# Performance work log

Measured on AMD Instinct MI355X. Metric: run time of the kernel, lower is better.

The kernel has to match this reference:

```python
import jax, jax.numpy as jnp
import numpy as np

N = 50000      # nodes
E = 800000     # edges
IN = 256       # in_feats
H = 128        # out_classes*2
OUT = 64       # out_classes
ALPHA = 0.3


def setup_inputs() -> dict:
    key = jax.random.key(0)
    ks = jax.random.split(key, 12)
    x = jax.random.normal(ks[0], (N, IN), jnp.float32)
    edge_index = jax.random.randint(ks[1], (2, E), 0, N, dtype=jnp.int32)
    def lin(k, fi, fo):
        s = 1.0 / np.float32(np.sqrt(fi))
        kw, kb = jax.random.split(k)
        return (jax.random.uniform(kw, (fi, fo), jnp.float32, -s, s),
                jax.random.uniform(kb, (fo,), jnp.float32, -s, s))
    W1, b1 = lin(ks[2], IN, H)
    W2, b2 = lin(ks[3], H, H)
    W3, b3 = lin(ks[4], H, H)
    Wfc, bfc = lin(ks[5], H, OUT)
    jk_weights = jax.random.normal(ks[6], (3,), jnp.float32)
    return dict(x=x, edge_index=edge_index, W1=W1, b1=b1, W2=W2, b2=b2,
                W3=W3, b3=b3, jk_weights=jk_weights, Wfc=Wfc, bfc=bfc)


def _gcn(x, W, b, src, dst, norm, n):
    # symmetric-normalized GCN conv with self-loops folded into src/dst/norm
    h = x @ W
    return jax.ops.segment_sum(norm[:, None] * h[src], dst, num_segments=n) + b


def reference(x, edge_index, W1, b1, W2, b2, W3, b3, jk_weights, Wfc, bfc):
    n = x.shape[0]
    row, col = edge_index[0], edge_index[1]
    loops = jnp.arange(n, dtype=edge_index.dtype)
    src = jnp.concatenate([row, loops])
    dst = jnp.concatenate([col, loops])
    deg = jax.ops.segment_sum(jnp.ones(src.shape, jnp.float32), dst, num_segments=n)
    dinv = jax.lax.rsqrt(jnp.maximum(deg, 1.0))  # deg >= 1 due to self-loops
    norm = dinv[src] * dinv[dst]

    layer_out = []
    # layer 0 + neighbor sampling (defaults make it exact out-neighbor mean)
    h = jax.nn.relu(_gcn(x, W1, b1, src, dst, norm, n))
    odeg = jax.ops.segment_sum(jnp.ones(row.shape, jnp.float32), row, num_segments=n)
    nsum = jax.ops.segment_sum(h[col], row, num_segments=n)
    h = jnp.where(odeg[:, None] > 0, nsum / jnp.maximum(odeg, 1.0)[:, None], h)
    layer_out.append(h)

    # layer 1 + historical EMA (fresh hist = detached x -> value identity, grad*alpha)
    h = jax.nn.relu(_gcn(h, W2, b2, src, dst, norm, n))
    sg = jax.lax.stop_gradient(h)
    h = sg + ALPHA * (h - sg)
    layer_out.append(h)

    # layer 2
    h = jax.nn.relu(_gcn(h, W3, b3, src, dst, norm, n))
    layer_out.append(h)

    w = jax.nn.softmax(jk_weights)
    jk = w[0] * layer_out[0] + w[1] * layer_out[1] + w[2] * layer_out[2]
    return jk @ Wfc + bfc
```

## Files before the change

### kernel.cpp

```cpp
#include <hip/hip_runtime.h>
#include <hip/hip_bf16.h>


#define H_FEATS 128

typedef __attribute__((ext_vector_type(8))) short short8;
typedef __attribute__((ext_vector_type(4))) float float4v;
typedef unsigned short u16;

__device__ __forceinline__ float dload(const void* p, size_t i, int isbf) {
    return isbf ? __bfloat162float(((const __hip_bfloat16*)p)[i])
                : ((const float*)p)[i];
}

__device__ __forceinline__ float4 load4bf(const u16* p) {
    uint2 u = *(const uint2*)p;
    float4 f;
    f.x = __uint_as_float((u.x & 0xFFFFu) << 16);
    f.y = __uint_as_float(u.x & 0xFFFF0000u);
    f.z = __uint_as_float((u.y & 0xFFFFu) << 16);
    f.w = __uint_as_float(u.y & 0xFFFF0000u);
    return f;
}

__device__ __forceinline__ float bf2f(u16 h) {
    return __uint_as_float((unsigned)h << 16);
}

__device__ __forceinline__ u16 f2bf(float v) {
    return __bfloat16_as_ushort(__float2bfloat16(v));
}

__device__ __forceinline__ void sniff_body(const unsigned int* __restrict__ x,
                                           const void* __restrict__ jkwb,
                                           float* __restrict__ meta) {
    __shared__ int cnt[256];
    int t = threadIdx.x;
    int c = 0;
    for (int i = 0; i < 16; i++) {
        unsigned int w = x[t * 16 + i];
        unsigned int e = (w >> 7) & 0xFFu;
        c += (e >= 0x60u && e <= 0x8Fu) ? 1 : 0;
    }
    cnt[t] = c;
    __syncthreads();
    for (int s = 128; s > 0; s >>= 1) {
        if (t < s) cnt[t] += cnt[t + s];
        __syncthreads();
    }
    if (t == 0) {
        int isbf = (cnt[0] > 3000) ? 1 : 0;
        ((int*)meta)[0] = isbf;
        float w0 = dload(jkwb, 0, isbf);
        float w1 = dload(jkwb, 1, isbf);
        float w2 = dload(jkwb, 2, isbf);
        float m = fmaxf(w0, fmaxf(w1, w2));
        float e0 = expf(w0 - m), e1 = expf(w1 - m), e2 = expf(w2 - m);
        float s = e0 + e1 + e2;
        meta[8] = e0 / s; meta[9] = e1 / s; meta[10] = e2 / s;
    }
}

__global__ __launch_bounds__(256) void sniff_jkw(const unsigned int* __restrict__ x,
                                                 const void* __restrict__ jkwb,
                                                 float* __restrict__ meta) {
    sniff_body(x, jkwb, meta);
}


#define CSR_CH 64
#define CSR_SL 8
#define CSR_NSC (CSR_CH * CSR_SL * 2)

__global__ __launch_bounds__(256) void count_partial(const int* __restrict__ row,
                                                     const int* __restrict__ col,
                                                     unsigned* __restrict__ partC,
                                                     unsigned* __restrict__ partR,
                                                     int E, int N,
                                                     const unsigned int* __restrict__ x,
                                                     const void* __restrict__ jkwb,
                                                     float* __restrict__ meta) {
    if (blockIdx.x == gridDim.x - 1) {
        sniff_body(x, jkwb, meta);
        return;
    }
    int b = blockIdx.x;
    int dir = b >> 9;
    int r = b & 511;
    int sl = r >> 6;
    int k  = r & 63;
    const int* arr = dir ? row : col;
    unsigned* part = (dir ? partR : partC) + (size_t)k * N;
    int lo = (int)(((long long)N * sl) >> 3);
    int hi = (int)(((long long)N * (sl + 1)) >> 3);
    int wid = hi - lo;

    __shared__ unsigned cnt[8192];
    for (int i = threadIdx.x; i < wid; i += 256) cnt[i] = 0;
    __syncthreads();

    int e0 = (int)(((long long)E * k) >> 6);
    int e1 = (int)(((long long)E * (k + 1)) >> 6);
    for (int e = e0 + threadIdx.x; e < e1; e += 256) {
        int d = arr[e] - lo;
        if ((unsigned)d < (unsigned)wid) atomicAdd(&cnt[d], 1u);
    }
    __syncthreads();
    for (int i = threadIdx.x; i < wid; i += 256) part[lo + i] = cnt[i];
}

__global__ __launch_bounds__(256) void reduce_bsum(const unsigned* __restrict__ partC,
                                                   const unsigned* __restrict__ partR,
                                                   int* __restrict__ cntc,
                                                   int* __restrict__ cntr,
                                                   int* __restrict__ b0,
                                                   int* __restrict__ b1, int N) {
    const unsigned* p = blockIdx.y ? partR : partC;
    int* cnt = blockIdx.y ? cntr : cntc;
    int* bs = blockIdx.y ? b1 : b0;
    int base = blockIdx.x * 1024 + threadIdx.x * 4;
    unsigned v0 = 0, v1 = 0, v2 = 0, v3 = 0;
    if (base + 3 < N) {
        for (int k = 0; k < CSR_CH; k++) {
            uint4 u = *(const uint4*)(p + (size_t)k * N + base);
            v0 += u.x; v1 += u.y; v2 += u.z; v3 += u.w;
        }
        int4 w = {(int)v0, (int)v1, (int)v2, (int)v3};
        *(int4*)&cnt[base] = w;
    } else {
        unsigned vv[4] = {0, 0, 0, 0};
        for (int k = 0; k < CSR_CH; k++)
            for (int i = 0; i < 4; i++)
                if (base + i < N) vv[i] += p[(size_t)k * N + base + i];
        for (int i = 0; i < 4; i++) if (base + i < N) cnt[base + i] = (int)vv[i];
        v0 = vv[0]; v1 = vv[1]; v2 = vv[2]; v3 = vv[3];
    }
    int s = (int)(v0 + v1 + v2 + v3);
    __shared__ int red[256];
    red[threadIdx.x] = s;
    __syncthreads();
    for (int d = 128; d > 0; d >>= 1) {
        if (threadIdx.x < d) red[threadIdx.x] += red[threadIdx.x + d];
        __syncthreads();
    }
    if (threadIdx.x == 0) bs[blockIdx.x] = red[0];
}

__global__ __launch_bounds__(256) void prefix_partials(unsigned* __restrict__ partC,
                                                       unsigned* __restrict__ partR,
                                                       const int* __restrict__ coff,
                                                       const int* __restrict__ roff, int N) {
    int i = blockIdx.x * 256 + threadIdx.x;
    if (i >= N) return;
    unsigned* p = blockIdx.y ? partR : partC;
    const int* off = blockIdx.y ? roff : coff;
    unsigned acc = (unsigned)off[i];
    for (int k = 0; k < CSR_CH; k++) {
        unsigned t = p[(size_t)k * N + i];
        p[(size_t)k * N + i] = acc;
        acc += t;
    }
}

__device__ __forceinline__ void scatter_body(int b,
                                             const int* __restrict__ row,
                                             const int* __restrict__ col,
                                             const unsigned* __restrict__ partC,
                                             const unsigned* __restrict__ partR,
                                             u16* __restrict__ ecol,
                                             u16* __restrict__ erow,
                                             int E, int N,
                                             unsigned* __restrict__ cur) {
    int dir = b >> 9;
    int r = b & 511;
    int sl = r >> 6;
    int k  = r & 63;
    const int* darr = dir ? row : col;
    const int* sarr = dir ? col : row;
    u16* out = dir ? erow : ecol;
    const unsigned* base = (dir ? partR : partC) + (size_t)k * N;
    int lo = (int)(((long long)N * sl) >> 3);
    int hi = (int)(((long long)N * (sl + 1)) >> 3);
    int wid = hi - lo;

    for (int i = threadIdx.x; i < wid; i += 256) cur[i] = base[lo + i];
    __syncthreads();

    int e0 = (int)(((long long)E * k) >> 6);
    int e1 = (int)(((long long)E * (k + 1)) >> 6);
    for (int e = e0 + threadIdx.x; e < e1; e += 256) {
        int d = darr[e] - lo;
        if ((unsigned)d < (unsigned)wid) {
            unsigned p = atomicAdd(&cur[d], 1u);
            out[p] = (u16)sarr[e];
        }
    }
}

__global__ __launch_bounds__(256) void histo_sniff(const int* __restrict__ row, const int* __restrict__ col,
                                                   int* __restrict__ cntc, int* __restrict__ cntr, int E,
                                                   const unsigned int* __restrict__ x,
                                                   const void* __restrict__ jkwb,
                                                   float* __restrict__ meta) {
    if (blockIdx.x == gridDim.x - 1) {
        sniff_body(x, jkwb, meta);
        return;
    }
    int e = blockIdx.x * 256 + threadIdx.x;
    if (e < E) {
        atomicAdd(&cntc[col[e]], 1);
        atomicAdd(&cntr[row[e]], 1);
    }
}

__global__ __launch_bounds__(256) void scan_bsum(const int* __restrict__ c0, const int* __restrict__ c1,
                                                 int* __restrict__ b0, int* __restrict__ b1, int N) {
    const int* cnt = blockIdx.y ? c1 : c0;
    int* bs = blockIdx.y ? b1 : b0;
    int base = blockIdx.x * 1024 + threadIdx.x * 4;
    int s = 0;
    if (base + 3 < N) {
        int4 v = *(const int4*)&cnt[base];
        s = v.x + v.y + v.z + v.w;
    } else {
        for (int i = 0; i < 4; i++) if (base + i < N) s += cnt[base + i];
    }
    __shared__ int red[256];
    red[threadIdx.x] = s;
    __syncthreads();
    for (int d = 128; d > 0; d >>= 1) {
        if (threadIdx.x < d) red[threadIdx.x] += red[threadIdx.x + d];
        __syncthreads();
    }
    if (threadIdx.x == 0) bs[blockIdx.x] = red[0];
}

__global__ __launch_bounds__(256) void scan_bsum_scan(int* __restrict__ b0, int* __restrict__ b1,
                                                      int* __restrict__ offN0, int* __restrict__ offN1,
                                                      int nb) {
    int* bs = blockIdx.x ? b1 : b0;
    int* offN = blockIdx.x ? offN1 : offN0;
    __shared__ int sh[256];
    int t = threadIdx.x;
    int v = (t < nb) ? bs[t] : 0;
    sh[t] = v;
    __syncthreads();
    for (int d = 1; d < 256; d <<= 1) {
        int u = (t >= d) ? sh[t - d] : 0;
        __syncthreads();
        sh[t] += u;
        __syncthreads();
    }
    if (t < nb) bs[t] = (t == 0) ? 0 : sh[t - 1];
    if (t == 255) *offN = sh[255];
}

__global__ __launch_bounds__(256) void scan_final(const int* __restrict__ c0, const int* __restrict__ c1,
                                                  const int* __restrict__ b0, const int* __restrict__ b1,
                                                  int* __restrict__ o0, int* __restrict__ u0,
                                                  int* __restrict__ o1, int* __restrict__ u1,
                                                  float* __restrict__ dinvp, int N) {
    const int* cnt = blockIdx.y ? c1 : c0;
    const int* bs  = blockIdx.y ? b1 : b0;
    int* off = blockIdx.y ? o1 : o0;
    int* cur = blockIdx.y ? u1 : u0;
    int t = threadIdx.x;
    int base = blockIdx.x * 1024 + t * 4;
    int4 v = {0, 0, 0, 0};
    if (base + 3 < N) {
        v = *(const int4*)&cnt[base];
    } else {
        int tmp[4] = {0, 0, 0, 0};
        for (int i = 0; i < 4; i++) if (base + i < N) tmp[i] = cnt[base + i];
        v.x = tmp[0]; v.y = tmp[1]; v.z = tmp[2]; v.w = tmp[3];
    }
    if (blockIdx.y == 0) {
        if (base + 3 < N) {
            float4 dv;
            dv.x = rsqrtf(1.0f + (float)v.x);
            dv.y = rsqrtf(1.0f + (float)v.y);
            dv.z = rsqrtf(1.0f + (float)v.z);
            dv.w = rsqrtf(1.0f + (float)v.w);
            *(float4*)&dinvp[base] = dv;
        } else {
            int vv[4] = {v.x, v.y, v.z, v.w};
            for (int i = 0; i < 4; i++)
                if (base + i < N) dinvp[base + i] = rsqrtf(1.0f + (float)vv[i]);
        }
    }
    int s = v.x + v.y + v.z + v.w;
    __shared__ int sh[256];
    sh[t] = s;
    __syncthreads();
    for (int d = 1; d < 256; d <<= 1) {
        int u = (t >= d) ? sh[t - d] : 0;
        __syncthreads();
        sh[t] += u;
        __syncthreads();
    }
    int ex = bs[blockIdx.x] + ((t == 0) ? 0 : sh[t - 1]);
    int4 o;
    o.x = ex; o.y = ex + v.x; o.z = o.y + v.y; o.w = o.z + v.z;
    if (base + 3 < N) {
        *(int4*)&off[base] = o;
        *(int4*)&cur[base] = o;
    } else {
        int arr[4] = {o.x, o.y, o.z, o.w};
        for (int i = 0; i < 4; i++) if (base + i < N) { off[base + i] = arr[i]; cur[base + i] = arr[i]; }
    }
}

__global__ __launch_bounds__(256) void scatter_tile(const int* __restrict__ row, const int* __restrict__ col,
                                                    int* __restrict__ curc, int* __restrict__ curr,
                                                    u16* __restrict__ ecol, u16* __restrict__ erow,
                                                    int E, int lo, int hi, int doRow) {
    int e = blockIdx.x * 256 + threadIdx.x;
    if (e >= E) return;
    int s = row[e], d = col[e];
    if (d >= lo && d < hi) {
        int p = atomicAdd(&curc[d], 1);
        ecol[p] = (u16)s;
    }
    if (doRow && s >= lo && s < hi) {
        int q = atomicAdd(&curr[s], 1);
        erow[q] = (u16)d;
    }
}

__global__ __launch_bounds__(256) void pack_all(const void* __restrict__ W1,
                                                const void* __restrict__ W2,
                                                const void* __restrict__ W3,
                                                u16* __restrict__ Wp1,
                                                u16* __restrict__ Wp2,
                                                u16* __restrict__ Wp3,
                                                const int* __restrict__ flagp) {
    int bid = blockIdx.x;
    const void* W; u16* Wp; int K, gid;
    if (bid < 16)      { W = W1; Wp = Wp1; K = 256; gid = bid * 256 + threadIdx.x; }
    else if (bid < 24) { W = W2; Wp = Wp2; K = 128; gid = (bid - 16) * 256 + threadIdx.x; }
    else               { W = W3; Wp = Wp3; K = 128; gid = (bid - 24) * 256 + threadIdx.x; }
    int steps = K >> 5;
    if (gid >= steps * 8 * 64) return;
    int isbf = *flagp;
    int lane = gid & 63;
    int t = (gid >> 6) & 7;
    int s = gid >> 9;
    int krow = s * 32 + ((lane >> 4) << 3);
    int ncol = t * 16 + (lane & 15);
#pragma unroll
    for (int j = 0; j < 8; j++) {
        float v = dload(W, (size_t)(krow + j) * H_FEATS + ncol, isbf);
        Wp[(size_t)gid * 8 + j] = f2bf(v);
    }
}

template <int K, bool RTBF, bool BFIN, bool SCALE>
__device__ __forceinline__ void gemm_mfma_body(int bid, const void* __restrict__ Xv,
                                               const u16* __restrict__ Wp,
                                               u16* __restrict__ Cb,
                                               const float* __restrict__ dinv,
                                               const int* __restrict__ flagp, int M) {
    const int isbf = RTBF ? *flagp : (BFIN ? 1 : 0);
    const int tid = threadIdx.x;
    const int wave = tid >> 6, lane = tid & 63;
    const int m16 = lane & 15, quad = lane >> 4;
    const int row = bid * 64 + wave * 16 + m16;
    constexpr int STEPS = K / 32;

    float4v acc[8];
#pragma unroll
    for (int t = 0; t < 8; t++) acc[t] = (float4v){0.f, 0.f, 0.f, 0.f};

    const bool rowOK = row < M;
#pragma unroll
    for (int s = 0; s < STEPS; s++) {
        int k0 = s * 32 + quad * 8;
        short8 a = (short8)(short)0;
        if (rowOK) {
            if (isbf) {
                a = *(const short8*)((const u16*)Xv + (size_t)row * K + k0);
            } else {
                const float* p = (const float*)Xv + (size_t)row * K + k0;
                float4 f0 = *(const float4*)p;
                float4 f1 = *(const float4*)(p + 4);
                a[0] = (short)f2bf(f0.x); a[1] = (short)f2bf(f0.y);
                a[2] = (short)f2bf(f0.z); a[3] = (short)f2bf(f0.w);
                a[4] = (short)f2bf(f1.x); a[5] = (short)f2bf(f1.y);
                a[6] = (short)f2bf(f1.z); a[7] = (short)f2bf(f1.w);
            }
        }
#pragma unroll
        for (int t = 0; t < 8; t++) {
            short8 b = *(const short8*)(Wp + ((size_t)(s * 8 + t) * 64 + lane) * 8);
            acc[t] = __builtin_amdgcn_mfma_f32_16x16x32_bf16(a, b, acc[t], 0, 0, 0);
        }
    }
#pragma unroll
    for (int r = 0; r < 4; r++) {
        int gr = bid * 64 + wave * 16 + quad * 4 + r;
        if (gr < M) {
            float sc = SCALE ? dinv[gr] : 1.0f;
#pragma unroll
            for (int t = 0; t < 8; t++) {
                size_t o = (size_t)gr * H_FEATS + t * 16 + m16;
                Cb[o] = f2bf(sc * acc[t][r]);
            }
        }
    }
}

template <int K, bool RTBF, bool BFIN, bool SCALE>
__global__ __launch_bounds__(256) void gemm_mfma(const void* __restrict__ Xv,
                                                 const u16* __restrict__ Wp,
                                                 u16* __restrict__ Cb,
                                                 const float* __restrict__ dinv,
                                                 const int* __restrict__ flagp, int M) {
    gemm_mfma_body<K, RTBF, BFIN, SCALE>(blockIdx.x, Xv, Wp, Cb, dinv, flagp, M);
}

__global__ __launch_bounds__(256) void scatter_gemm0(const int* __restrict__ row,
                                                     const int* __restrict__ col,
                                                     const unsigned* __restrict__ partC,
                                                     const unsigned* __restrict__ partR,
                                                     u16* __restrict__ ecol,
                                                     u16* __restrict__ erow,
                                                     int E, int N,
                                                     const void* __restrict__ Xv,
                                                     const u16* __restrict__ Wp,
                                                     u16* __restrict__ Pb,
                                                     const float* __restrict__ dinv,
                                                     const int* __restrict__ flagp) {
    __shared__ unsigned cur[8192];
    if (blockIdx.x < CSR_NSC) {
        scatter_body(blockIdx.x, row, col, partC, partR, ecol, erow, E, N, cur);
    } else {
        gemm_mfma_body<256, true, false, true>(blockIdx.x - CSR_NSC, Xv, Wp, Pb, dinv, flagp, N);
    }
}

__global__ __launch_bounds__(256) void agg_sum(const int* __restrict__ off,
                                               const u16* __restrict__ idx,
                                               const float* __restrict__ dinv,
                                               const u16* __restrict__ Pb,
                                               const void* __restrict__ bv,
                                               u16* __restrict__ hout,
                                               const int* __restrict__ flagp, int N) {
    int node = blockIdx.x * 8 + (threadIdx.x >> 5);
    if (node >= N) return;
    int l = threadIdx.x & 31;
    int isbf = *flagp;
    int beg = off[node], end = off[node + 1];
    size_t ro = (size_t)l * 4;

    float4 acc = load4bf(&Pb[(size_t)node * H_FEATS + ro]);

    const float4 z = {0.f, 0.f, 0.f, 0.f};
    int i = beg;
    int s0 = (i     < end) ? (int)idx[i]     : 0;
    int s1 = (i + 1 < end) ? (int)idx[i + 1] : 0;
    int s2 = (i + 2 < end) ? (int)idx[i + 2] : 0;
    int s3 = (i + 3 < end) ? (int)idx[i + 3] : 0;
    float4 h0 = (i     < end) ? load4bf(&Pb[(size_t)s0 * H_FEATS + ro]) : z;
    float4 h1 = (i + 1 < end) ? load4bf(&Pb[(size_t)s1 * H_FEATS + ro]) : z;
    float4 h2 = (i + 2 < end) ? load4bf(&Pb[(size_t)s2 * H_FEATS + ro]) : z;
    float4 h3 = (i + 3 < end) ? load4bf(&Pb[(size_t)s3 * H_FEATS + ro]) : z;
    for (; i + 4 < end; i += 4) {
        int t0 = (int)idx[i + 4];
        int t1 = (i + 5 < end) ? (int)idx[i + 5] : 0;
        int t2 = (i + 6 < end) ? (int)idx[i + 6] : 0;
        int t3 = (i + 7 < end) ? (int)idx[i + 7] : 0;
        float4 n0 = load4bf(&Pb[(size_t)t0 * H_FEATS + ro]);
        float4 n1 = (i + 5 < end) ? load4bf(&Pb[(size_t)t1 * H_FEATS + ro]) : z;
        float4 n2 = (i + 6 < end) ? load4bf(&Pb[(size_t)t2 * H_FEATS + ro]) : z;
        float4 n3 = (i + 7 < end) ? load4bf(&Pb[(size_t)t3 * H_FEATS + ro]) : z;
        acc.x += (h0.x + h1.x) + (h2.x + h3.x);
        acc.y += (h0.y + h1.y) + (h2.y + h3.y);
        acc.z += (h0.z + h1.z) + (h2.z + h3.z);
        acc.w += (h0.w + h1.w) + (h2.w + h3.w);
        h0 = n0; h1 = n1; h2 = n2; h3 = n3;
    }
    acc.x += (h0.x + h1.x) + (h2.x + h3.x);
    acc.y += (h0.y + h1.y) + (h2.y + h3.y);
    acc.z += (h0.z + h1.z) + (h2.z + h3.z);
    acc.w += (h0.w + h1.w) + (h2.w + h3.w);

    float dd = dinv[node];
    acc.x = fmaxf(fmaf(dd, acc.x, dload(bv, l * 4 + 0, isbf)), 0.0f);
    acc.y = fmaxf(fmaf(dd, acc.y, dload(bv, l * 4 + 1, isbf)), 0.0f);
    acc.z = fmaxf(fmaf(dd, acc.z, dload(bv, l * 4 + 2, isbf)), 0.0f);
    acc.w = fmaxf(fmaf(dd, acc.w, dload(bv, l * 4 + 3, isbf)), 0.0f);
    uint2 pk;
    pk.x = (unsigned)f2bf(acc.x) | ((unsigned)f2bf(acc.y) << 16);
    pk.y = (unsigned)f2bf(acc.z) | ((unsigned)f2bf(acc.w) << 16);
    *(uint2*)&hout[(size_t)node * H_FEATS + ro] = pk;
}

__global__ __launch_bounds__(256) void mean_gather3b(const int* __restrict__ off,
                                                     const u16* __restrict__ idx,
                                                     const u16* __restrict__ Hb,
                                                     u16* __restrict__ hout, int N) {
    int node = blockIdx.x * 8 + (threadIdx.x >> 5);
    if (node >= N) return;
    int l = threadIdx.x & 31;
    int beg = off[node], end = off[node + 1];
    size_t ro = (size_t)l * 4;

    const float4 z = {0.f, 0.f, 0.f, 0.f};
    float4 acc = z;
    int i = beg;
    int s0 = (i     < end) ? (int)idx[i]     : 0;
    int s1 = (i + 1 < end) ? (int)idx[i + 1] : 0;
    int s2 = (i + 2 < end) ? (int)idx[i + 2] : 0;
    int s3 = (i + 3 < end) ? (int)idx[i + 3] : 0;
    float4 h0 = (i     < end) ? load4bf(&Hb[(size_t)s0 * H_FEATS + ro]) : z;
    float4 h1 = (i + 1 < end) ? load4bf(&Hb[(size_t)s1 * H_FEATS + ro]) : z;
    float4 h2 = (i + 2 < end) ? load4bf(&Hb[(size_t)s2 * H_FEATS + ro]) : z;
    float4 h3 = (i + 3 < end) ? load4bf(&Hb[(size_t)s3 * H_FEATS + ro]) : z;
    for (; i + 4 < end; i += 4) {
        int t0 = (int)idx[i + 4];
        int t1 = (i + 5 < end) ? (int)idx[i + 5] : 0;
        int t2 = (i + 6 < end) ? (int)idx[i + 6] : 0;
        int t3 = (i + 7 < end) ? (int)idx[i + 7] : 0;
        float4 n0 = load4bf(&Hb[(size_t)t0 * H_FEATS + ro]);
        float4 n1 = (i + 5 < end) ? load4bf(&Hb[(size_t)t1 * H_FEATS + ro]) : z;
        float4 n2 = (i + 6 < end) ? load4bf(&Hb[(size_t)t2 * H_FEATS + ro]) : z;
        float4 n3 = (i + 7 < end) ? load4bf(&Hb[(size_t)t3 * H_FEATS + ro]) : z;
        acc.x += (h0.x + h1.x) + (h2.x + h3.x);
        acc.y += (h0.y + h1.y) + (h2.y + h3.y);
        acc.z += (h0.z + h1.z) + (h2.z + h3.z);
        acc.w += (h0.w + h1.w) + (h2.w + h3.w);
        h0 = n0; h1 = n1; h2 = n2; h3 = n3;
    }
    acc.x += (h0.x + h1.x) + (h2.x + h3.x);
    acc.y += (h0.y + h1.y) + (h2.y + h3.y);
    acc.z += (h0.z + h1.z) + (h2.z + h3.z);
    acc.w += (h0.w + h1.w) + (h2.w + h3.w);

    int cnt = end - beg;
    float4 res;
    if (cnt > 0) {
        float inv = 1.0f / (float)cnt;
        res.x = acc.x * inv; res.y = acc.y * inv; res.z = acc.z * inv; res.w = acc.w * inv;
    } else {
        res = load4bf(&Hb[(size_t)node * H_FEATS + ro]);
    }
    uint2 pk;
    pk.x = (unsigned)f2bf(res.x) | ((unsigned)f2bf(res.y) << 16);
    pk.y = (unsigned)f2bf(res.z) | ((unsigned)f2bf(res.w) << 16);
    *(uint2*)&hout[(size_t)node * H_FEATS + ro] = pk;
}

template <bool BF16OUT>
__global__ __launch_bounds__(256) void agg_gather3b(const int* __restrict__ off,
                                                    const u16* __restrict__ idx,
                                                    const float* __restrict__ dinv,
                                                    const u16* __restrict__ Hb,
                                                    const void* __restrict__ bv,
                                                    void* __restrict__ houtv,
                                                    const int* __restrict__ flagp, int N) {
    int node = blockIdx.x * 8 + (threadIdx.x >> 5);
    if (node >= N) return;
    int l = threadIdx.x & 31;
    int isbf = *flagp;
    int beg = off[node], end = off[node + 1];
    float dd = dinv[node];
    size_t ro = (size_t)l * 4;

    float4 self = load4bf(&Hb[(size_t)node * H_FEATS + ro]);
    float w0s = dd * dd;
    float4 acc = {w0s * self.x, w0s * self.y, w0s * self.z, w0s * self.w};

    int i = beg;
    int s0 = (i < end) ? (int)idx[i] : 0;
    float4 h0 = (i < end) ? load4bf(&Hb[(size_t)s0 * H_FEATS + ro])
                          : (float4){0.f, 0.f, 0.f, 0.f};
    for (; i < end; i++) {
        int s1 = (i + 1 < end) ? (int)idx[i + 1] : 0;
        float4 h1 = (i + 1 < end) ? load4bf(&Hb[(size_t)s1 * H_FEATS + ro]) : h0;
        float w = dinv[s0] * dd;
        acc.x = fmaf(w, h0.x, acc.x);
        acc.y = fmaf(w, h0.y, acc.y);
        acc.z = fmaf(w, h0.z, acc.z);
        acc.w = fmaf(w, h0.w, acc.w);
        s0 = s1; h0 = h1;
    }
    acc.x = fmaxf(acc.x + dload(bv, l * 4 + 0, isbf), 0.0f);
    acc.y = fmaxf(acc.y + dload(bv, l * 4 + 1, isbf), 0.0f);
    acc.z = fmaxf(acc.z + dload(bv, l * 4 + 2, isbf), 0.0f);
    acc.w = fmaxf(acc.w + dload(bv, l * 4 + 3, isbf), 0.0f);
    if (BF16OUT) {
        u16* hb = (u16*)houtv;
        uint2 pk;
        pk.x = (unsigned)f2bf(acc.x) | ((unsigned)f2bf(acc.y) << 16);
        pk.y = (unsigned)f2bf(acc.z) | ((unsigned)f2bf(acc.w) << 16);
        *(uint2*)&hb[(size_t)node * H_FEATS + ro] = pk;
    } else {
        *(float4*)&((float*)houtv)[(size_t)node * H_FEATS + ro] = acc;
    }
}

__global__ __launch_bounds__(256) void fc3(const u16* __restrict__ H0,
                                           const u16* __restrict__ H1,
                                           const u16* __restrict__ H2,
                                           const void* __restrict__ Wv,
                                           const void* __restrict__ bv,
                                           void* __restrict__ Outv,
                                           const float* __restrict__ meta, int N) {
    constexpr int BM = 64, BK = 16, BN = 64, TN = 4, TX = BN / TN, K = 128;
    __shared__ float Xs[BK][BM + 4];
    __shared__ float Ws[BK][BN];
    const int isbf = ((const int*)meta)[0];
    const float w0 = meta[8], w1 = meta[9], w2 = meta[10];

    const int tid = threadIdx.x;
    const int tx = tid % TX;
    const int ty = tid / TX;
    const int rowBase = blockIdx.x * BM;

    float acc[4][TN] = {};
    const int lk = tid % BK;
    const int lr0 = tid / BK;

    for (int kb = 0; kb < K; kb += BK) {
#pragma unroll
        for (int i = 0; i < 4; i++) {
            int r = lr0 + i * 16;
            int gr = rowBase + r;
            float v = 0.0f;
            if (gr < N) {
                size_t idx = (size_t)gr * K + kb + lk;
                v = w0 * bf2f(H0[idx]) + w1 * bf2f(H1[idx]) + w2 * bf2f(H2[idx]);
            }
            Xs[lk][r] = v;
        }
#pragma unroll
        for (int i = 0; i < 4; i++) {
            int idx = i * 256 + tid;
            int k = idx >> 6, c = idx & 63;
            Ws[k][c] = dload(Wv, (size_t)(kb + k) * BN + c, isbf);
        }
        __syncthreads();
#pragma unroll
        for (int k = 0; k < BK; k++) {
            float4 a = *(const float4*)&Xs[k][ty * 4];
            float av[4] = {a.x, a.y, a.z, a.w};
            float4 bb = *(const float4*)&Ws[k][tx * TN];
            float bvv[4] = {bb.x, bb.y, bb.z, bb.w};
#pragma unroll
            for (int i = 0; i < 4; i++)
#pragma unroll
                for (int j = 0; j < TN; j++) acc[i][j] = fmaf(av[i], bvv[j], acc[i][j]);
        }
        __syncthreads();
    }
    __hip_bfloat16* ob = (__hip_bfloat16*)Outv;
    float* of = (float*)Outv;
#pragma unroll
    for (int i = 0; i < 4; i++) {
        int gr = rowBase + ty * 4 + i;
        if (gr < N) {
#pragma unroll
            for (int j = 0; j < TN; j++) {
                int c = tx * TN + j;
                size_t o = (size_t)gr * BN + c;
                float v = acc[i][j] + dload(bv, c, isbf);
                if (isbf) ob[o] = __float2bfloat16(v); else of[o] = v;
            }
        }
    }
}

template <int K, bool XIN, bool GATEBF, bool BF16OUT>
__global__ __launch_bounds__(256) void gemm128(const void* __restrict__ Xv,
                                               const void* __restrict__ Wv,
                                               void* __restrict__ Cv,
                                               const int* __restrict__ flagp, int N) {
    constexpr int BM = 64, BK = 16, BN = 128, TN = 8, TX = BN / TN;
    __shared__ float Xs[BK][BM + 4];
    __shared__ float Ws[BK][BN];
    const int isbf = *flagp;
    if (GATEBF && isbf != 1) return;
    const float* Xf = (const float*)Xv;

    const int tid = threadIdx.x;
    const int tx = tid % TX;
    const int ty = tid / TX;
    const int rowBase = blockIdx.x * BM;

    float acc[4][TN] = {};
    const int lk = tid % BK;
    const int lr0 = tid / BK;

    for (int kb = 0; kb < K; kb += BK) {
#pragma unroll
        for (int i = 0; i < 4; i++) {
            int r = lr0 + i * 16;
            int gr = rowBase + r;
            float v = 0.0f;
            if (gr < N) {
                size_t idx = (size_t)gr * K + kb + lk;
                v = XIN ? dload(Xv, idx, isbf) : Xf[idx];
            }
            Xs[lk][r] = v;
        }
#pragma unroll
        for (int i = 0; i < 8; i++) {
            int idx = i * 256 + tid;
            int k = idx >> 7, c = idx & 127;
            Ws[k][c] = dload(Wv, (size_t)(kb + k) * BN + c, isbf);
        }
        __syncthreads();
#pragma unroll
        for (int k = 0; k < BK; k++) {
            float4 a = *(const float4*)&Xs[k][ty * 4];
            float av[4] = {a.x, a.y, a.z, a.w};
            float4 b0 = *(const float4*)&Ws[k][tx * TN];
            float4 b1 = *(const float4*)&Ws[k][tx * TN + 4];
            float bv[8] = {b0.x, b0.y, b0.z, b0.w, b1.x, b1.y, b1.z, b1.w};
#pragma unroll
            for (int i = 0; i < 4; i++)
#pragma unroll
                for (int j = 0; j < TN; j++) acc[i][j] = fmaf(av[i], bv[j], acc[i][j]);
        }
        __syncthreads();
    }
#pragma unroll
    for (int i = 0; i < 4; i++) {
        int gr = rowBase + ty * 4 + i;
        if (gr < N) {
#pragma unroll
            for (int j = 0; j < TN; j++) {
                size_t o = (size_t)gr * BN + tx * TN + j;
                if (BF16OUT) ((u16*)Cv)[o] = f2bf(acc[i][j]);
                else         ((float*)Cv)[o] = acc[i][j];
            }
        }
    }
}

template <bool FIRST, bool LAST, bool BFIN>
__global__ __launch_bounds__(256) void fc_accum(const void* __restrict__ Hmv,
                                                const void* __restrict__ Wv,
                                                const void* __restrict__ bv,
                                                void* __restrict__ Outv,
                                                const float* __restrict__ meta,
                                                int widx, int N) {
    constexpr int BM = 64, BK = 16, BN = 64, TN = 4, TX = BN / TN, K = 128;
    __shared__ float Xs[BK][BM + 4];
    __shared__ float Ws[BK][BN];
    const int isbf = ((const int*)meta)[0];
    const float scale = meta[8 + widx];

    const int tid = threadIdx.x;
    const int tx = tid % TX;
    const int ty = tid / TX;
    const int rowBase = blockIdx.x * BM;

    float acc[4][TN] = {};
    const int lk = tid % BK;
    const int lr0 = tid / BK;

    for (int kb = 0; kb < K; kb += BK) {
#pragma unroll
        for (int i = 0; i < 4; i++) {
            int r = lr0 + i * 16;
            int gr = rowBase + r;
            float v = 0.0f;
            if (gr < N) {
                size_t idx = (size_t)gr * K + kb + lk;
                if (BFIN) v = bf2f(((const u16*)Hmv)[idx]);
                else      v = ((const float*)Hmv)[idx];
            }
            Xs[lk][r] = v;
        }
#pragma unroll
        for (int i = 0; i < 4; i++) {
            int idx = i * 256 + tid;
            int k = idx >> 6, c = idx & 63;
            Ws[k][c] = dload(Wv, (size_t)(kb + k) * BN + c, isbf);
        }
        __syncthreads();
#pragma unroll
        for (int k = 0; k < BK; k++) {
            float4 a = *(const float4*)&Xs[k][ty * 4];
            float av[4] = {a.x, a.y, a.z, a.w};
            float4 bb = *(const float4*)&Ws[k][tx * TN];
            float bvv[4] = {bb.x, bb.y, bb.z, bb.w};
#pragma unroll
            for (int i = 0; i < 4; i++)
#pragma unroll
                for (int j = 0; j < TN; j++) acc[i][j] = fmaf(av[i], bvv[j], acc[i][j]);
        }
        __syncthreads();
    }
    __hip_bfloat16* ob = (__hip_bfloat16*)Outv;
    float* of = (float*)Outv;
#pragma unroll
    for (int i = 0; i < 4; i++) {
        int gr = rowBase + ty * 4 + i;
        if (gr < N) {
#pragma unroll
            for (int j = 0; j < TN; j++) {
                int c = tx * TN + j;
                size_t o = (size_t)gr * BN + c;
                float v = scale * acc[i][j];
                if (!FIRST) v += isbf ? __bfloat162float(ob[o]) : of[o];
                if (LAST) v += dload(bv, c, isbf);
                if (isbf) ob[o] = __float2bfloat16(v); else of[o] = v;
            }
        }
    }
}

__global__ __launch_bounds__(256) void init_deg(float* deg, float* odeg, int N) {
    int i = blockIdx.x * 256 + threadIdx.x;
    if (i < N) { deg[i] = 1.0f; odeg[i] = 0.0f; }
}
__global__ __launch_bounds__(256) void count_deg(const int* __restrict__ row, const int* __restrict__ col,
                                                 float* deg, float* odeg, int E) {
    int e = blockIdx.x * 256 + threadIdx.x;
    if (e < E) {
        atomicAdd(&deg[col[e]], 1.0f);
        atomicAdd(&odeg[row[e]], 1.0f);
    }
}
__global__ __launch_bounds__(256) void deg_to_dinv(float* deg, int N) {
    int i = blockIdx.x * 256 + threadIdx.x;
    if (i < N) deg[i] = rsqrtf(deg[i]);
}
__global__ __launch_bounds__(256) void agg_edges(const int* __restrict__ row, const int* __restrict__ col,
                                                 const float* __restrict__ dinv,
                                                 const float* __restrict__ H,
                                                 float* __restrict__ agg, int E) {
    int e = blockIdx.x * 2 + (threadIdx.x >> 7);
    if (e >= E) return;
    int j = threadIdx.x & 127;
    int s = row[e], d = col[e];
    float w = dinv[s] * dinv[d];
    atomicAdd(&agg[(size_t)d * H_FEATS + j], w * H[(size_t)s * H_FEATS + j]);
}
__global__ __launch_bounds__(256) void mean_edges(const int* __restrict__ row, const int* __restrict__ col,
                                                  const float* __restrict__ h0pre,
                                                  float* __restrict__ nsum, int E) {
    int e = blockIdx.x * 2 + (threadIdx.x >> 7);
    if (e >= E) return;
    int j = threadIdx.x & 127;
    int r = row[e], c = col[e];
    atomicAdd(&nsum[(size_t)r * H_FEATS + j], h0pre[(size_t)c * H_FEATS + j]);
}
__global__ __launch_bounds__(256) void finalize_layer(const float* __restrict__ agg,
                                                      const float* __restrict__ H,
                                                      const float* __restrict__ dinv,
                                                      const void* __restrict__ bv,
                                                      float* __restrict__ hout,
                                                      const int* __restrict__ flagp, int NH) {
    int idx = blockIdx.x * 256 + threadIdx.x;
    if (idx >= NH) return;
    int isbf = *flagp;
    int v = idx >> 7, j = idx & 127;
    float di = dinv[v];
    float h = fmaf(di * di, H[idx], agg[idx]) + dload(bv, j, isbf);
    hout[idx] = fmaxf(h, 0.0f);
}
__global__ __launch_bounds__(256) void finalize_mean(const float* __restrict__ nsum,
                                                     const float* __restrict__ h0pre,
                                                     const float* __restrict__ odeg,
                                                     float* __restrict__ h0, int NH) {
    int idx = blockIdx.x * 256 + threadIdx.x;
    if (idx >= NH) return;
    int v = idx >> 7;
    float od = odeg[v];
    h0[idx] = (od > 0.0f) ? (nsum[idx] / od) : h0pre[idx];
}
__global__ __launch_bounds__(256) void finalize_mean_cnt(const float* __restrict__ nsum,
                                                         const float* __restrict__ h0pre,
                                                         const int* __restrict__ cntr,
                                                         float* __restrict__ h0, int NH) {
    int idx = blockIdx.x * 256 + threadIdx.x;
    if (idx >= NH) return;
    int v = idx >> 7;
    int od = cntr[v];
    h0[idx] = (od > 0) ? (nsum[idx] / (float)od) : h0pre[idx];
}

extern "C" void kernel_launch(void* const* d_in, const int* in_sizes, int n_in,
                              void* d_out, int out_size, void* d_ws, size_t ws_size,
                              hipStream_t stream) {
    const void* x   = d_in[0];
    const int*  ei  = (const int*)d_in[1];
    const void* W1  = d_in[2];
    const void* b1  = d_in[3];
    const void* W2  = d_in[4];
    const void* b2  = d_in[5];
    const void* W3  = d_in[6];
    const void* b3  = d_in[7];
    const void* jkb = d_in[8];
    const void* Wfc = d_in[9];
    const void* bfc = d_in[10];

    const int IN = 256;
    const int N = in_sizes[0] / IN;
    const int E = in_sizes[1] / 2;
    const int NH = N * H_FEATS;

    const int* row = ei;
    const int* col = ei + E;

    auto a4 = [](size_t v) { return (v + 3) & ~(size_t)3; };
    float* ws = (float*)d_ws;
    size_t o = 0;
    float* meta  = ws + o;           o += 256;
    float* dinv  = ws + o;           o += N;          o = a4(o);
    int*   cntc  = (int*)(ws + o);   o += N;          o = a4(o);
    int*   cntr  = (int*)(ws + o);   o += N;          o = a4(o);
    int*   bsumc = (int*)(ws + o);   o += 256;
    int*   bsumr = (int*)(ws + o);   o += 256;
    int*   coff  = (int*)(ws + o);   o += N + 1;      o = a4(o);
    int*   curc  = (int*)(ws + o);   o += N;          o = a4(o);
    u16*   ecol  = (u16*)(ws + o);   o += E;          o = a4(o);
    size_t oB_small = o;
    int*   roff  = (int*)(ws + o);   o += N + 1;      o = a4(o);
    int*   curr  = (int*)(ws + o);   o += N;          o = a4(o);
    u16*   erow  = (u16*)(ws + o);   o += E;          o = a4(o);
    size_t oA_full = o;

    auto alignup = [](size_t v) { return (v + 63) & ~(size_t)63; };
    const size_t WPW = 16384 + 8192 + 8192;
    size_t needA = alignup(oA_full) + 2 * (size_t)NH + 64 + WPW;
    size_t needB = alignup(oB_small) + 2 * (size_t)NH + 64 + WPW;

    int tier;
    size_t hoff;
    if (N >= 65536)                { tier = 2; hoff = alignup(256 + 2 * (size_t)N); }
    else if (ws_size >= needA * 4) { tier = 0; hoff = alignup(oA_full); }
    else if (ws_size >= needB * 4) { tier = 1; hoff = alignup(oB_small); }
    else                           { tier = 2; hoff = alignup(256 + 2 * (size_t)N); }
    float* A = ws + hoff;
    float* B = A + NH;
    u16* HbA = (u16*)A;
    u16* HbB = (u16*)B;
    u16* Pb  = (u16*)A;
    u16* Qb  = Pb + (size_t)NH;
    u16* H0b = Pb + 2 * (size_t)NH;
    u16* H1b = Pb + 3 * (size_t)NH;
    unsigned* partC = (unsigned*)H0b;
    unsigned* partR = partC + (size_t)CSR_CH * N;
    size_t wpoff = alignup(hoff + 2 * (size_t)NH);
    u16* Wp1 = (u16*)(ws + wpoff);
    u16* Wp2 = Wp1 + 32768;
    u16* Wp3 = Wp2 + 16384;
    float* odegf = ws + 256 + N;
    const int* flag = (const int*)meta;

    dim3 blk(256);
    int gN = (N + 255) / 256;
    int gE = (E + 255) / 256;
    int gE2 = (E + 1) / 2;
    int gNH = (NH + 255) / 256;
    int gGemm = (N + 63) / 64;
    int gNode8 = (N + 7) / 8;
    int nb = (N + 1023) / 1024;

    if (tier == 0) {
        count_partial<<<CSR_NSC + 1, blk, 0, stream>>>(row, col, partC, partR, E, N,
                                                       (const unsigned int*)x, jkb, meta);
        pack_all<<<32, blk, 0, stream>>>(W1, W2, W3, Wp1, Wp2, Wp3, flag);
        reduce_bsum<<<dim3(nb, 2), blk, 0, stream>>>(partC, partR, cntc, cntr, bsumc, bsumr, N);
        scan_bsum_scan<<<2, blk, 0, stream>>>(bsumc, bsumr, &coff[N], &roff[N], nb);
        scan_final<<<dim3(nb, 2), blk, 0, stream>>>(cntc, cntr, bsumc, bsumr,
                                                    coff, curc, roff, curr, dinv, N);
        prefix_partials<<<dim3(gN, 2), blk, 0, stream>>>(partC, partR, coff, roff, N);

        scatter_gemm0<<<CSR_NSC + gGemm, blk, 0, stream>>>(row, col, partC, partR, ecol, erow,
                                                           E, N, x, Wp1, Pb, dinv, flag);

        agg_sum<<<gNode8, blk, 0, stream>>>(coff, ecol, dinv, Pb, b1, Qb, flag, N);
        mean_gather3b<<<gNode8, blk, 0, stream>>>(roff, erow, Qb, H0b, N);

        gemm_mfma<128, false, true, true><<<gGemm, blk, 0, stream>>>(H0b, Wp2, Pb, dinv, flag, N);
        agg_sum<<<gNode8, blk, 0, stream>>>(coff, ecol, dinv, Pb, b2, H1b, flag, N);

        gemm_mfma<128, false, true, true><<<gGemm, blk, 0, stream>>>(H1b, Wp3, Pb, dinv, flag, N);
        agg_sum<<<gNode8, blk, 0, stream>>>(coff, ecol, dinv, Pb, b3, Qb, flag, N);

        fc3<<<gGemm, blk, 0, stream>>>(H0b, H1b, Qb, Wfc, bfc, d_out, meta, N);
    } else if (tier == 1) {
        hipMemsetAsync(cntc, 0, 2 * (size_t)N * 4, stream);
        histo_sniff<<<gE + 1, blk, 0, stream>>>(row, col, cntc, cntr, E,
                                                (const unsigned int*)x, jkb, meta);
        const int T = 4;
        int step = (N + T - 1) / T;
        scan_bsum<<<dim3(nb, 1), blk, 0, stream>>>(cntc, cntc, bsumc, bsumc, N);
        scan_bsum_scan<<<1, blk, 0, stream>>>(bsumc, bsumc, &coff[N], &coff[N], nb);
        scan_final<<<dim3(nb, 1), blk, 0, stream>>>(cntc, cntc, bsumc, bsumc,
                                                    coff, curc, coff, curc, dinv, N);
        for (int t = 0; t < T; t++) {
            int lo = t * step, hi = lo + step; if (hi > N) hi = N;
            scatter_tile<<<gE, blk, 0, stream>>>(row, col, curc, curc, ecol, ecol, E, lo, hi, 0);
        }

        pack_all<<<32, blk, 0, stream>>>(W1, W2, W3, Wp1, Wp2, Wp3, flag);

        gemm_mfma<256, true, false, false><<<gGemm, blk, 0, stream>>>(x, Wp1, HbA, dinv, flag, N);
        agg_gather3b<false><<<gNode8, blk, 0, stream>>>(coff, ecol, dinv, HbA, b1, B, flag, N);
        hipMemsetAsync(A, 0, (size_t)NH * 4, stream);
        mean_edges<<<gE2, blk, 0, stream>>>(row, col, B, A, E);
        finalize_mean_cnt<<<gNH, blk, 0, stream>>>(A, B, cntr, A, NH);
        fc_accum<true, false, false><<<gGemm, blk, 0, stream>>>(A, Wfc, bfc, d_out, meta, 0, N);

        gemm_mfma<128, false, false, false><<<gGemm, blk, 0, stream>>>(A, Wp2, HbB, dinv, flag, N);
        agg_gather3b<true><<<gNode8, blk, 0, stream>>>(coff, ecol, dinv, HbB, b2, HbA, flag, N);
        fc_accum<false, false, true><<<gGemm, blk, 0, stream>>>(HbA, Wfc, bfc, d_out, meta, 1, N);

        gemm_mfma<128, false, true, false><<<gGemm, blk, 0, stream>>>(HbA, Wp3, HbB, dinv, flag, N);
        agg_gather3b<true><<<gNode8, blk, 0, stream>>>(coff, ecol, dinv, HbB, b3, HbA, flag, N);
        fc_accum<false, true, true><<<gGemm, blk, 0, stream>>>(HbA, Wfc, bfc, d_out, meta, 2, N);
    } else {
        sniff_jkw<<<1, blk, 0, stream>>>((const unsigned int*)x, jkb, meta);
        init_deg<<<gN, blk, 0, stream>>>(dinv, odegf, N);
        count_deg<<<gE, blk, 0, stream>>>(row, col, dinv, odegf, E);
        deg_to_dinv<<<gN, blk, 0, stream>>>(dinv, N);

        gemm128<256, true, false, false><<<gGemm, blk, 0, stream>>>(x, W1, A, flag, N);
        hipMemsetAsync(B, 0, (size_t)NH * 4, stream);
        agg_edges<<<gE2, blk, 0, stream>>>(row, col, dinv, A, B, E);
        finalize_layer<<<gNH, blk, 0, stream>>>(B, A, dinv, b1, B, flag, NH);
        hipMemsetAsync(A, 0, (size_t)NH * 4, stream);
        mean_edges<<<gE2, blk, 0, stream>>>(row, col, B, A, E);
        finalize_mean<<<gNH, blk, 0, stream>>>(A, B, odegf, A, NH);
        fc_accum<true, false, false><<<gGemm, blk, 0, stream>>>(A, Wfc, bfc, d_out, meta, 0, N);

        gemm128<128, false, false, false><<<gGemm, blk, 0, stream>>>(A, W2, B, flag, N);
        hipMemsetAsync(A, 0, (size_t)NH * 4, stream);
        agg_edges<<<gE2, blk, 0, stream>>>(row, col, dinv, B, A, E);
        finalize_layer<<<gNH, blk, 0, stream>>>(A, B, dinv, b2, A, flag, NH);
        fc_accum<false, false, false><<<gGemm, blk, 0, stream>>>(A, Wfc, bfc, d_out, meta, 1, N);

        gemm128<128, false, false, false><<<gGemm, blk, 0, stream>>>(A, W3, B, flag, N);
        hipMemsetAsync(A, 0, (size_t)NH * 4, stream);
        agg_edges<<<gE2, blk, 0, stream>>>(row, col, dinv, B, A, E);
        finalize_layer<<<gNH, blk, 0, stream>>>(A, B, dinv, b3, A, flag, NH);
        fc_accum<false, true, false><<<gGemm, blk, 0, stream>>>(A, Wfc, bfc, d_out, meta, 2, N);
    }
}
```

Baseline: 460.7 us.

## Fuse neighbor gather with following MFMA GEMM and final FC via LDS tiles

The mean-gather and the per-layer aggregations now write each block's 64-row output tile into LDS, then immediately run the next layer's MFMA GEMM (or the final JK-weighted FC) on that tile inside the same kernel. This removes separate gemm_mfma and fc3 launches and one global round trip of the intermediate features per layer. Gather now uses 16 lanes per row with 16-byte loads instead of 32 lanes with 8-byte loads. In exchange, each block handles 64 rows serially across passes, which lowers parallelism for latency-bound gathers, and the LDS tile use may reduce occupancy.

```diff
diff --git a/kernel.cpp b/kernel.cpp
--- a/kernel.cpp
+++ b/kernel.cpp
@@ -3,6 +3,7 @@
 
 
 #define H_FEATS 128
+#define TPAD 136
 
 typedef __attribute__((ext_vector_type(8))) short short8;
 typedef __attribute__((ext_vector_type(4))) float float4v;
@@ -29,6 +30,37 @@
 
 __device__ __forceinline__ u16 f2bf(float v) {
     return __bfloat16_as_ushort(__float2bfloat16(v));
+}
+
+__device__ __forceinline__ void add8(float* a, uint4 u) {
+    a[0] += __uint_as_float((u.x & 0xFFFFu) << 16);
+    a[1] += __uint_as_float(u.x & 0xFFFF0000u);
+    a[2] += __uint_as_float((u.y & 0xFFFFu) << 16);
+    a[3] += __uint_as_float(u.y & 0xFFFF0000u);
+    a[4] += __uint_as_float((u.z & 0xFFFFu) << 16);
+    a[5] += __uint_as_float(u.z & 0xFFFF0000u);
+    a[6] += __uint_as_float((u.w & 0xFFFFu) << 16);
+    a[7] += __uint_as_float(u.w & 0xFFFF0000u);
+}
+
+__device__ __forceinline__ void set8(float* a, uint4 u) {
+    a[0] = __uint_as_float((u.x & 0xFFFFu) << 16);
+    a[1] = __uint_as_float(u.x & 0xFFFF0000u);
+    a[2] = __uint_as_float((u.y & 0xFFFFu) << 16);
+    a[3] = __uint_as_float(u.y & 0xFFFF0000u);
+    a[4] = __uint_as_float((u.z & 0xFFFFu) << 16);
+    a[5] = __uint_as_float(u.z & 0xFFFF0000u);
+    a[6] = __uint_as_float((u.w & 0xFFFFu) << 16);
+    a[7] = __uint_as_float(u.w & 0xFFFF0000u);
+}
+
+__device__ __forceinline__ uint4 pack8(const float* f) {
+    uint4 r;
+    r.x = (unsigned)f2bf(f[0]) | ((unsigned)f2bf(f[1]) << 16);
+    r.y = (unsigned)f2bf(f[2]) | ((unsigned)f2bf(f[3]) << 16);
+    r.z = (unsigned)f2bf(f[4]) | ((unsigned)f2bf(f[5]) << 16);
+    r.w = (unsigned)f2bf(f[6]) | ((unsigned)f2bf(f[7]) << 16);
+    return r;
 }
 
 __device__ __forceinline__ void sniff_body(const unsigned int* __restrict__ x,
@@ -66,7 +98,6 @@
                                                  float* __restrict__ meta) {
     sniff_body(x, jkwb, meta);
 }
-
 
 #define CSR_CH 64
 #define CSR_SL 8
@@ -495,59 +526,208 @@
     *(uint2*)&hout[(size_t)node * H_FEATS + ro] = pk;
 }
 
-__global__ __launch_bounds__(256) void mean_gather3b(const int* __restrict__ off,
-                                                     const u16* __restrict__ idx,
-                                                     const u16* __restrict__ Hb,
-                                                     u16* __restrict__ hout, int N) {
-    int node = blockIdx.x * 8 + (threadIdx.x >> 5);
-    if (node >= N) return;
-    int l = threadIdx.x & 31;
-    int beg = off[node], end = off[node + 1];
-    size_t ro = (size_t)l * 4;
-
-    const float4 z = {0.f, 0.f, 0.f, 0.f};
-    float4 acc = z;
-    int i = beg;
-    int s0 = (i     < end) ? (int)idx[i]     : 0;
-    int s1 = (i + 1 < end) ? (int)idx[i + 1] : 0;
-    int s2 = (i + 2 < end) ? (int)idx[i + 2] : 0;
-    int s3 = (i + 3 < end) ? (int)idx[i + 3] : 0;
-    float4 h0 = (i     < end) ? load4bf(&Hb[(size_t)s0 * H_FEATS + ro]) : z;
-    float4 h1 = (i + 1 < end) ? load4bf(&Hb[(size_t)s1 * H_FEATS + ro]) : z;
-    float4 h2 = (i + 2 < end) ? load4bf(&Hb[(size_t)s2 * H_FEATS + ro]) : z;
-    float4 h3 = (i + 3 < end) ? load4bf(&Hb[(size_t)s3 * H_FEATS + ro]) : z;
-    for (; i + 4 < end; i += 4) {
-        int t0 = (int)idx[i + 4];
-        int t1 = (i + 5 < end) ? (int)idx[i + 5] : 0;
-        int t2 = (i + 6 < end) ? (int)idx[i + 6] : 0;
-        int t3 = (i + 7 < end) ? (int)idx[i + 7] : 0;
-        float4 n0 = load4bf(&Hb[(size_t)t0 * H_FEATS + ro]);
-        float4 n1 = (i + 5 < end) ? load4bf(&Hb[(size_t)t1 * H_FEATS + ro]) : z;
-        float4 n2 = (i + 6 < end) ? load4bf(&Hb[(size_t)t2 * H_FEATS + ro]) : z;
-        float4 n3 = (i + 7 < end) ? load4bf(&Hb[(size_t)t3 * H_FEATS + ro]) : z;
-        acc.x += (h0.x + h1.x) + (h2.x + h3.x);
-        acc.y += (h0.y + h1.y) + (h2.y + h3.y);
-        acc.z += (h0.z + h1.z) + (h2.z + h3.z);
-        acc.w += (h0.w + h1.w) + (h2.w + h3.w);
-        h0 = n0; h1 = n1; h2 = n2; h3 = n3;
-    }
-    acc.x += (h0.x + h1.x) + (h2.x + h3.x);
-    acc.y += (h0.y + h1.y) + (h2.y + h3.y);
-    acc.z += (h0.z + h1.z) + (h2.z + h3.z);
-    acc.w += (h0.w + h1.w) + (h2.w + h3.w);
-
-    int cnt = end - beg;
-    float4 res;
-    if (cnt > 0) {
-        float inv = 1.0f / (float)cnt;
-        res.x = acc.x * inv; res.y = acc.y * inv; res.z = acc.z * inv; res.w = acc.w * inv;
-    } else {
-        res = load4bf(&Hb[(size_t)node * H_FEATS + ro]);
-    }
-    uint2 pk;
-    pk.x = (unsigned)f2bf(res.x) | ((unsigned)f2bf(res.y) << 16);
-    pk.y = (unsigned)f2bf(res.z) | ((unsigned)f2bf(res.w) << 16);
-    *(uint2*)&hout[(size_t)node * H_FEATS + ro] = pk;
+template <int MODE, bool WRITEG>
+__device__ __forceinline__ void gather_tile(int bid,
+                                            const int* __restrict__ off,
+                                            const u16* __restrict__ idx,
+                                            const float* __restrict__ dinv,
+                                            const u16* __restrict__ Src,
+                                            const void* __restrict__ bv, int isbf,
+                                            u16* __restrict__ Hg,
+                                            u16* __restrict__ tile, int N) {
+    int lane16 = threadIdx.x & 15;
+    int rloc = threadIdx.x >> 4;
+    int co = lane16 * 8;
+    const uint4 zz = {0u, 0u, 0u, 0u};
+#pragma unroll
+    for (int pass = 0; pass < 4; ++pass) {
+        int r = pass * 16 + rloc;
+        int gr = bid * 64 + r;
+        uint4* ldst = (uint4*)(tile + (size_t)r * TPAD + co);
+        if (gr >= N) { *ldst = zz; continue; }
+        int beg = off[gr], end = off[gr + 1];
+        float acc[8];
+        if (MODE == 0) {
+            uint4 u = *(const uint4*)(Src + (size_t)gr * H_FEATS + co);
+            set8(acc, u);
+        } else {
+#pragma unroll
+            for (int j = 0; j < 8; j++) acc[j] = 0.0f;
+        }
+        int i = beg;
+        int s0 = (i     < end) ? (int)idx[i]     : 0;
+        int s1 = (i + 1 < end) ? (int)idx[i + 1] : 0;
+        int s2 = (i + 2 < end) ? (int)idx[i + 2] : 0;
+        int s3 = (i + 3 < end) ? (int)idx[i + 3] : 0;
+        uint4 h0 = (i     < end) ? *(const uint4*)(Src + (size_t)s0 * H_FEATS + co) : zz;
+        uint4 h1 = (i + 1 < end) ? *(const uint4*)(Src + (size_t)s1 * H_FEATS + co) : zz;
+        uint4 h2 = (i + 2 < end) ? *(const uint4*)(Src + (size_t)s2 * H_FEATS + co) : zz;
+        uint4 h3 = (i + 3 < end) ? *(const uint4*)(Src + (size_t)s3 * H_FEATS + co) : zz;
+        for (; i + 4 < end; i += 4) {
+            int t0 = (int)idx[i + 4];
+            int t1 = (i + 5 < end) ? (int)idx[i + 5] : 0;
+            int t2 = (i + 6 < end) ? (int)idx[i + 6] : 0;
+            int t3 = (i + 7 < end) ? (int)idx[i + 7] : 0;
+            uint4 n0 = *(const uint4*)(Src + (size_t)t0 * H_FEATS + co);
+            uint4 n1 = (i + 5 < end) ? *(const uint4*)(Src + (size_t)t1 * H_FEATS + co) : zz;
+            uint4 n2 = (i + 6 < end) ? *(const uint4*)(Src + (size_t)t2 * H_FEATS + co) : zz;
+            uint4 n3 = (i + 7 < end) ? *(const uint4*)(Src + (size_t)t3 * H_FEATS + co) : zz;
+            add8(acc, h0); add8(acc, h1); add8(acc, h2); add8(acc, h3);
+            h0 = n0; h1 = n1; h2 = n2; h3 = n3;
+        }
+        add8(acc, h0); add8(acc, h1); add8(acc, h2); add8(acc, h3);
+
+        if (MODE == 0) {
+            float dd = dinv[gr];
+#pragma unroll
+            for (int j = 0; j < 8; j++)
+                acc[j] = fmaxf(fmaf(dd, acc[j], dload(bv, co + j, isbf)), 0.0f);
+        } else {
+            int cnt = end - beg;
+            if (cnt > 0) {
+                float inv = 1.0f / (float)cnt;
+#pragma unroll
+                for (int j = 0; j < 8; j++) acc[j] *= inv;
+            } else {
+                uint4 u = *(const uint4*)(Src + (size_t)gr * H_FEATS + co);
+                set8(acc, u);
+            }
+        }
+        uint4 pk = pack8(acc);
+        *ldst = pk;
+        if (WRITEG) *(uint4*)(Hg + (size_t)gr * H_FEATS + co) = pk;
+    }
+}
+
+__device__ __forceinline__ void gemm_lds_body(int bid, const u16* __restrict__ tile,
+                                              const u16* __restrict__ Wp,
+                                              u16* __restrict__ Cb,
+                                              const float* __restrict__ dinv, int M) {
+    const int tid = threadIdx.x;
+    const int wave = tid >> 6, lane = tid & 63;
+    const int m16 = lane & 15, quad = lane >> 4;
+    const int lrow = wave * 16 + m16;
+
+    float4v acc[8];
+#pragma unroll
+    for (int t = 0; t < 8; t++) acc[t] = (float4v){0.f, 0.f, 0.f, 0.f};
+
+#pragma unroll
+    for (int s = 0; s < 4; s++) {
+        int k0 = s * 32 + quad * 8;
+        short8 a = *(const short8*)(tile + (size_t)lrow * TPAD + k0);
+#pragma unroll
+        for (int t = 0; t < 8; t++) {
+            short8 b = *(const short8*)(Wp + ((size_t)(s * 8 + t) * 64 + lane) * 8);
+            acc[t] = __builtin_amdgcn_mfma_f32_16x16x32_bf16(a, b, acc[t], 0, 0, 0);
+        }
+    }
+#pragma unroll
+    for (int r = 0; r < 4; r++) {
+        int gr = bid * 64 + wave * 16 + quad * 4 + r;
+        if (gr < M) {
+            float sc = dinv[gr];
+#pragma unroll
+            for (int t = 0; t < 8; t++) {
+                size_t o = (size_t)gr * H_FEATS + t * 16 + m16;
+                Cb[o] = f2bf(sc * acc[t][r]);
+            }
+        }
+    }
+}
+
+template <int MODE>
+__global__ __launch_bounds__(256) void agg_gemm(const int* __restrict__ off,
+                                                const u16* __restrict__ idx,
+                                                const float* __restrict__ dinv,
+                                                const u16* __restrict__ Src,
+                                                const void* __restrict__ bv,
+                                                const u16* __restrict__ Wp,
+                                                u16* __restrict__ Hg,
+                                                u16* __restrict__ Pnext,
+                                                const int* __restrict__ flagp, int N) {
+    __shared__ u16 tile[64 * TPAD];
+    gather_tile<MODE, true>(blockIdx.x, off, idx, dinv, Src, bv, *flagp, Hg, tile, N);
+    __syncthreads();
+    gemm_lds_body(blockIdx.x, tile, Wp, Pnext, dinv, N);
+}
+
+__global__ __launch_bounds__(256) void agg_fc3(const int* __restrict__ off,
+                                               const u16* __restrict__ idx,
+                                               const float* __restrict__ dinv,
+                                               const u16* __restrict__ Src,
+                                               const void* __restrict__ bv3,
+                                               const u16* __restrict__ H0,
+                                               const u16* __restrict__ H1,
+                                               const void* __restrict__ Wv,
+                                               const void* __restrict__ bv,
+                                               void* __restrict__ Outv,
+                                               const float* __restrict__ meta, int N) {
+    __shared__ u16 tile[64 * TPAD];
+    __shared__ float Xs[16][68];
+    __shared__ float Ws[16][64];
+    const int isbf = ((const int*)meta)[0];
+    gather_tile<0, false>(blockIdx.x, off, idx, dinv, Src, bv3, isbf, (u16*)0, tile, N);
+    __syncthreads();
+
+    const float w0 = meta[8], w1 = meta[9], w2 = meta[10];
+    const int tid = threadIdx.x;
+    const int tx = tid % 16;
+    const int ty = tid / 16;
+    const int rowBase = blockIdx.x * 64;
+
+    float acc[4][4] = {};
+    const int lk = tid % 16;
+    const int lr0 = tid / 16;
+
+    for (int kb = 0; kb < 128; kb += 16) {
+#pragma unroll
+        for (int i = 0; i < 4; i++) {
+            int r = lr0 + i * 16;
+            int gr = rowBase + r;
+            float v = 0.0f;
+            if (gr < N) {
+                size_t ix = (size_t)gr * H_FEATS + kb + lk;
+                v = w0 * bf2f(H0[ix]) + w1 * bf2f(H1[ix])
+                  + w2 * bf2f(tile[(size_t)r * TPAD + kb + lk]);
+            }
+            Xs[lk][r] = v;
+        }
+#pragma unroll
+        for (int i = 0; i < 4; i++) {
+            int ix = i * 256 + tid;
+            int k = ix >> 6, c = ix & 63;
+            Ws[k][c] = dload(Wv, (size_t)(kb + k) * 64 + c, isbf);
+        }
+        __syncthreads();
+#pragma unroll
+        for (int k = 0; k < 16; k++) {
+            float4 a = *(const float4*)&Xs[k][ty * 4];
+            float av[4] = {a.x, a.y, a.z, a.w};
+            float4 bb = *(const float4*)&Ws[k][tx * 4];
+            float bvv[4] = {bb.x, bb.y, bb.z, bb.w};
+#pragma unroll
+            for (int i = 0; i < 4; i++)
+#pragma unroll
+                for (int j = 0; j < 4; j++) acc[i][j] = fmaf(av[i], bvv[j], acc[i][j]);
+        }
+        __syncthreads();
+    }
+    __hip_bfloat16* ob = (__hip_bfloat16*)Outv;
+    float* of = (float*)Outv;
+#pragma unroll
+    for (int i = 0; i < 4; i++) {
+        int gr = rowBase + ty * 4 + i;
+        if (gr < N) {
+#pragma unroll
+            for (int j = 0; j < 4; j++) {
+                int c = tx * 4 + j;
+                size_t o = (size_t)gr * 64 + c;
+                float v = acc[i][j] + dload(bv, c, isbf);
+                if (isbf) ob[o] = __float2bfloat16(v); else of[o] = v;
+            }
+        }
+    }
 }
 
 template <bool BF16OUT>
@@ -596,77 +776,6 @@
         *(uint2*)&hb[(size_t)node * H_FEATS + ro] = pk;
     } else {
         *(float4*)&((float*)houtv)[(size_t)node * H_FEATS + ro] = acc;
-    }
-}
-
-__global__ __launch_bounds__(256) void fc3(const u16* __restrict__ H0,
-                                           const u16* __restrict__ H1,
-                                           const u16* __restrict__ H2,
-                                           const void* __restrict__ Wv,
-                                           const void* __restrict__ bv,
-                                           void* __restrict__ Outv,
-                                           const float* __restrict__ meta, int N) {
-    constexpr int BM = 64, BK = 16, BN = 64, TN = 4, TX = BN / TN, K = 128;
-    __shared__ float Xs[BK][BM + 4];
-    __shared__ float Ws[BK][BN];
-    const int isbf = ((const int*)meta)[0];
-    const float w0 = meta[8], w1 = meta[9], w2 = meta[10];
-
-    const int tid = threadIdx.x;
-    const int tx = tid % TX;
-    const int ty = tid / TX;
-    const int rowBase = blockIdx.x * BM;
-
-    float acc[4][TN] = {};
-    const int lk = tid % BK;
-    const int lr0 = tid / BK;
-
-    for (int kb = 0; kb < K; kb += BK) {
-#pragma unroll
-        for (int i = 0; i < 4; i++) {
-            int r = lr0 + i * 16;
-            int gr = rowBase + r;
-            float v = 0.0f;
-            if (gr < N) {
-                size_t idx = (size_t)gr * K + kb + lk;
-                v = w0 * bf2f(H0[idx]) + w1 * bf2f(H1[idx]) + w2 * bf2f(H2[idx]);
-            }
-            Xs[lk][r] = v;
-        }
-#pragma unroll
-        for (int i = 0; i < 4; i++) {
-            int idx = i * 256 + tid;
-            int k = idx >> 6, c = idx & 63;
-            Ws[k][c] = dload(Wv, (size_t)(kb + k) * BN + c, isbf);
-        }
-        __syncthreads();
-#pragma unroll
-        for (int k = 0; k < BK; k++) {
-            float4 a = *(const float4*)&Xs[k][ty * 4];
-            float av[4] = {a.x, a.y, a.z, a.w};
-            float4 bb = *(const float4*)&Ws[k][tx * TN];
-            float bvv[4] = {bb.x, bb.y, bb.z, bb.w};
-#pragma unroll
-            for (int i = 0; i < 4; i++)
-#pragma unroll
-                for (int j = 0; j < TN; j++) acc[i][j] = fmaf(av[i], bvv[j], acc[i][j]);
-        }
-        __syncthreads();
-    }
-    __hip_bfloat16* ob = (__hip_bfloat16*)Outv;
-    float* of = (float*)Outv;
-#pragma unroll
-    for (int i = 0; i < 4; i++) {
-        int gr = rowBase + ty * 4 + i;
-        if (gr < N) {
-#pragma unroll
-            for (int j = 0; j < TN; j++) {
-                int c = tx * TN + j;
-                size_t o = (size_t)gr * BN + c;
-                float v = acc[i][j] + dload(bv, c, isbf);
-                if (isbf) ob[o] = __float2bfloat16(v); else of[o] = v;
-            }
-        }
     }
 }
 
@@ -975,15 +1084,13 @@
                                                            E, N, x, Wp1, Pb, dinv, flag);
 
         agg_sum<<<gNode8, blk, 0, stream>>>(coff, ecol, dinv, Pb, b1, Qb, flag, N);
-        mean_gather3b<<<gNode8, blk, 0, stream>>>(roff, erow, Qb, H0b, N);
-
-        gemm_mfma<128, false, true, true><<<gGemm, blk, 0, stream>>>(H0b, Wp2, Pb, dinv, flag, N);
-        agg_sum<<<gNode8, blk, 0, stream>>>(coff, ecol, dinv, Pb, b2, H1b, flag, N);
-
-        gemm_mfma<128, false, true, true><<<gGemm, blk, 0, stream>>>(H1b, Wp3, Pb, dinv, flag, N);
-        agg_sum<<<gNode8, blk, 0, stream>>>(coff, ecol, dinv, Pb, b3, Qb, flag, N);
-
-        fc3<<<gGemm, blk, 0, stream>>>(H0b, H1b, Qb, Wfc, bfc, d_out, meta, N);
+
+        agg_gemm<1><<<gGemm, blk, 0, stream>>>(roff, erow, dinv, Qb, b1, Wp2, H0b, Pb, flag, N);
+
+        agg_gemm<0><<<gGemm, blk, 0, stream>>>(coff, ecol, dinv, Pb, b2, Wp3, H1b, Qb, flag, N);
+
+        agg_fc3<<<gGemm, blk, 0, stream>>>(coff, ecol, dinv, Qb, b3, H0b, H1b,
+                                           Wfc, bfc, d_out, meta, N);
     } else if (tier == 1) {
         hipMemsetAsync(cntc, 0, 2 * (size_t)N * 4, stream);
         histo_sniff<<<gE + 1, blk, 0, stream>>>(row, col, cntc, cntr, E,
```

Result: faster. 428.8 us (-6.9%).
